# Kernel optimization log

Hardware: AMD Instinct MI355X
Metric: run time of the kernel (lower is better)

## Reference

```python
import jax, jax.numpy as jnp
import numpy as np

N = 100_000      # nodes
E = 500_000      # edges
D = 128          # node_feature_dim
IN = 2 * D       # VAE in_features
H = 128          # hidden_ch
L = 5            # latent_features
V2 = 3.5
BETA = 10.0


def _init_linear(key, fan_in, fan_out):
    kw, kb = jax.random.split(key)
    bound = 1.0 / np.sqrt(fan_in)
    W = jax.random.uniform(kw, (fan_in, fan_out), jnp.float32, -bound, bound)
    b = jax.random.uniform(kb, (fan_out,), jnp.float32, -bound, bound)
    return W, b


def setup_inputs() -> dict:
    key = jax.random.key(0)
    ks = jax.random.split(key, 12)
    x = jax.random.normal(ks[0], (N, D), jnp.float32)
    row = jax.random.randint(ks[1], (E,), 0, N, jnp.int32)
    col = jax.random.randint(ks[2], (E,), 0, N, jnp.int32)
    eps = jax.random.normal(ks[3], (E, L), jnp.float32)
    # encoder FCBlock: IN -> H -> H -> H -> 2L (ReLU on hidden layers)
    eW0, eb0 = _init_linear(ks[4], IN, H)
    eW1, eb1 = _init_linear(ks[5], H, H)
    eW2, eb2 = _init_linear(ks[6], H, H)
    eW3, eb3 = _init_linear(ks[7], H, 2 * L)
    # decoder FCBlock: L -> H -> H -> H -> IN
    dW0, db0 = _init_linear(ks[8], L, H)
    dW1, db1 = _init_linear(ks[9], H, H)
    dW2, db2 = _init_linear(ks[10], H, H)
    dW3, db3 = _init_linear(ks[11], H, IN)
    return dict(x=x, row=row, col=col, eps=eps,
                eW0=eW0, eb0=eb0, eW1=eW1, eb1=eb1, eW2=eW2, eb2=eb2, eW3=eW3, eb3=eb3,
                dW0=dW0, db0=db0, dW1=dW1, db1=db1, dW2=dW2, db2=db2, dW3=dW3, db3=db3)


def _mlp(h, layers):
    # ReLU on all but the last layer (FCBlock)
    n = len(layers)
    for i, (W, b) in enumerate(layers):
        h = h @ W + b
        if i < n - 1:
            h = jax.nn.relu(h)
    return h


def reference(x, row, col, eps,
              eW0, eb0, eW1, eb1, eW2, eb2, eW3, eb3,
              dW0, db0, dW1, db1, dW2, db2, dW3, db3):
    # gather node pairs -> [E, 2D]
    pair = jnp.concatenate([x[row], x[col]], axis=1)
    enc = _mlp(pair, [(eW0, eb0), (eW1, eb1), (eW2, eb2), (eW3, eb3)])
    mu, logvars = jnp.split(enc, 2, axis=1)          # [E, L] each
    std = jnp.exp(0.5 * logvars)
    z = mu + eps * std                               # reparameterization
    recon = _mlp(z, [(dW0, db0), (dW1, db1), (dW2, db2), (dW3, db3)])
    recon_loss = jnp.sqrt(jnp.sum((recon - pair) ** 2, axis=1))  # [E]
    kl_loss = -0.5 * (1.0 + logvars - mu ** 2 - jnp.exp(logvars)) * BETA  # [E, L]
    edge_affinities = 1.0 / (1.0 + V2 * recon_loss)  # [E]
    return edge_affinities, recon_loss.mean(), kl_loss.mean()
```

## Files before the change

### kernel.cpp

```cpp
#include <hip/hip_runtime.h>
#include <hip/hip_bf16.h>

typedef unsigned short u16;
typedef __attribute__((ext_vector_type(8))) short bf16x8;
typedef __attribute__((ext_vector_type(4))) float f32x4;

#define NE 500000
#define NBLOCKS ((NE + 127) / 128)

#define WE0_U 0u
#define WE1_U 32768u
#define WE2_U 49152u
#define WE3_U 65536u
#define WD0_U 67584u
#define WD1_U 71680u
#define WD2_U 88064u
#define WD3_U 104448u
#define WEND_U 137216u
#define BIAS_F 68608u
#define BE0_F 0
#define BE1_F 128
#define BE2_F 256
#define BE3_F 384
#define BD0_F 400
#define BD1_F 528
#define BD2_F 656
#define BD3_F 784
#define NBIAS 1040
#define ACC_BYTE 278592u

__device__ __forceinline__ u16 f2bf(float f) {
  __hip_bfloat16 h = __float2bfloat16(f);
  u16 u;
  __builtin_memcpy(&u, &h, 2);
  return u;
}

__global__ void prep_kernel(const float* __restrict__ eW0, const float* __restrict__ eb0,
                            const float* __restrict__ eW1, const float* __restrict__ eb1,
                            const float* __restrict__ eW2, const float* __restrict__ eb2,
                            const float* __restrict__ eW3, const float* __restrict__ eb3,
                            const float* __restrict__ dW0, const float* __restrict__ db0,
                            const float* __restrict__ dW1, const float* __restrict__ db1,
                            const float* __restrict__ dW2, const float* __restrict__ db2,
                            const float* __restrict__ dW3, const float* __restrict__ db3,
                            u16* __restrict__ wsu) {
  int t = blockIdx.x * 256 + threadIdx.x;
  float* wsf = (float*)wsu;
  if (t < 32768) {
    int n = t >> 8, k = t & 255;
    wsu[WE0_U + n * 256 + k] = f2bf(eW0[k * 128 + n]);
  } else if (t < 49152) {
    int i = t - 32768, n = i >> 7, k = i & 127;
    wsu[WE1_U + n * 128 + k] = f2bf(eW1[k * 128 + n]);
  } else if (t < 65536) {
    int i = t - 49152, n = i >> 7, k = i & 127;
    wsu[WE2_U + n * 128 + k] = f2bf(eW2[k * 128 + n]);
  } else if (t < 67584) {
    int i = t - 65536, n = i >> 7, k = i & 127;
    wsu[WE3_U + n * 128 + k] = f2bf(n < 10 ? eW3[k * 10 + n] : 0.f);
  } else if (t < 71680) {
    int i = t - 67584, n = i >> 5, k = i & 31;
    wsu[WD0_U + n * 32 + k] = f2bf(k < 5 ? dW0[k * 128 + n] : 0.f);
  } else if (t < 88064) {
    int i = t - 71680, n = i >> 7, k = i & 127;
    wsu[WD1_U + n * 128 + k] = f2bf(dW1[k * 128 + n]);
  } else if (t < 104448) {
    int i = t - 88064, n = i >> 7, k = i & 127;
    wsu[WD2_U + n * 128 + k] = f2bf(dW2[k * 128 + n]);
  } else if (t < 137216) {
    int i = t - 104448, n = i >> 7, k = i & 127;
    wsu[WD3_U + n * 128 + k] = f2bf(dW3[k * 256 + n]);
  } else if (t < 137216 + NBIAS) {
    int i = t - 137216;
    float v;
    if (i < 128) v = eb0[i];
    else if (i < 256) v = eb1[i - 128];
    else if (i < 384) v = eb2[i - 256];
    else if (i < 400) v = (i - 384 < 10) ? eb3[i - 384] : 0.f;
    else if (i < 528) v = db0[i - 400];
    else if (i < 656) v = db1[i - 528];
    else if (i < 784) v = db2[i - 656];
    else v = db3[i - 784];
    wsf[BIAS_F + i] = v;
  } else if (t < 137216 + NBIAS + 2) {
    ((double*)((char*)wsu + ACC_BYTE))[t - 137216 - NBIAS] = 0.0;
  }
}

__device__ __forceinline__ bf16x8 ldA(const u16* buf, int row, int k) {
  int byte = (row * 256 + k * 2) ^ ((row & 7) << 4);
  return *(const bf16x8*)((const char*)buf + byte);
}

__device__ __forceinline__ void init_acc(f32x4 acc[2][8], const float* __restrict__ bias, int j) {
  #pragma unroll
  for (int n = 0; n < 8; ++n) {
    float b = bias[n * 16 + j];
    f32x4 v = {b, b, b, b};
    acc[0][n] = v;
    acc[1][n] = v;
  }
}

template<int LDW>
__device__ __forceinline__ void gemm_acc(const u16* __restrict__ inb, const u16* __restrict__ Wt,
                                         int k0, f32x4 acc[2][8], int rw, int g, int j) {
  #pragma unroll
  for (int kk = 0; kk < 4; ++kk) {
    int k = kk * 32 + g * 8;
    bf16x8 a0 = ldA(inb, rw + j, k);
    bf16x8 a1 = ldA(inb, rw + 16 + j, k);
    #pragma unroll
    for (int n = 0; n < 8; ++n) {
      bf16x8 b = *(const bf16x8*)(Wt + (n * 16 + j) * LDW + k0 + k);
      acc[0][n] = __builtin_amdgcn_mfma_f32_16x16x32_bf16(a0, b, acc[0][n], 0, 0, 0);
      acc[1][n] = __builtin_amdgcn_mfma_f32_16x16x32_bf16(a1, b, acc[1][n], 0, 0, 0);
    }
  }
}

__device__ __forceinline__ void store_act(const f32x4 acc[2][8], u16* outb, int rw, int g, int j,
                                          bool relu) {
  #pragma unroll
  for (int m = 0; m < 2; ++m)
    #pragma unroll
    for (int n = 0; n < 8; ++n)
      #pragma unroll
      for (int r = 0; r < 4; ++r) {
        float v = acc[m][n][r];
        if (relu) v = fmaxf(v, 0.f);
        int row = rw + m * 16 + g * 4 + r;
        int c = n * 16 + j;
        int byte = (row * 256 + c * 2) ^ ((row & 7) << 4);
        *(u16*)((char*)outb + byte) = f2bf(v);
      }
}

__device__ __forceinline__ void stage(const float* __restrict__ x, const int* __restrict__ idx,
                                      int e0, u16* buf, int tid) {
  int gg = tid >> 4;
  int jj = tid & 15;
  #pragma unroll
  for (int p = 0; p < 8; ++p) {
    int rl = p * 16 + gg;
    int e = e0 + rl;
    if (e >= NE) e = NE - 1;
    int node = idx[e];
    const f32x4* src = (const f32x4*)(x + (size_t)node * 128 + jj * 8);
    f32x4 v0 = src[0];
    f32x4 v1 = src[1];
    bf16x8 o;
    o[0] = (short)f2bf(v0[0]); o[1] = (short)f2bf(v0[1]);
    o[2] = (short)f2bf(v0[2]); o[3] = (short)f2bf(v0[3]);
    o[4] = (short)f2bf(v1[0]); o[5] = (short)f2bf(v1[1]);
    o[6] = (short)f2bf(v1[2]); o[7] = (short)f2bf(v1[3]);
    int byte = (rl * 256 + jj * 16) ^ ((rl & 7) << 4);
    *(bf16x8*)((char*)buf + byte) = o;
  }
}

__global__ __launch_bounds__(256, 2) void vae_kernel(
    const float* __restrict__ x, const int* __restrict__ rowi, const int* __restrict__ coli,
    const float* __restrict__ eps, const u16* __restrict__ wsu, double* __restrict__ accg,
    float* __restrict__ out) {
  __shared__ __align__(16) u16 bufA[128 * 128];
  __shared__ __align__(16) u16 bufB[128 * 128];
  __shared__ __align__(16) u16 zbuf[128 * 32];
  __shared__ float redr[4], redk[4];

  const float* wsf = (const float*)wsu;
  const int tid = threadIdx.x;
  const int lane = tid & 63;
  const int wave = tid >> 6;
  const int g = lane >> 4;
  const int j = lane & 15;
  const int rw = wave * 32;
  const int e0 = blockIdx.x * 128;

  for (int i = tid; i < 128 * 32; i += 256) zbuf[i] = 0;

  float kl_part = 0.f, rl_part = 0.f;
  f32x4 acc[2][8];

  stage(x, rowi, e0, bufA, tid);
  __syncthreads();
  init_acc(acc, wsf + BIAS_F + BE0_F, j);
  gemm_acc<256>(bufA, wsu + WE0_U, 0, acc, rw, g, j);
  __syncthreads();
  stage(x, coli, e0, bufA, tid);
  __syncthreads();
  gemm_acc<256>(bufA, wsu + WE0_U, 128, acc, rw, g, j);
  store_act(acc, bufB, rw, g, j, true);
  __syncthreads();

  init_acc(acc, wsf + BIAS_F + BE1_F, j);
  gemm_acc<128>(bufB, wsu + WE1_U, 0, acc, rw, g, j);
  store_act(acc, bufA, rw, g, j, true);
  __syncthreads();

  init_acc(acc, wsf + BIAS_F + BE2_F, j);
  gemm_acc<128>(bufA, wsu + WE2_U, 0, acc, rw, g, j);
  store_act(acc, bufB, rw, g, j, true);
  __syncthreads();

  f32x4 a3[2];
  {
    float b3 = wsf[BIAS_F + BE3_F + j];
    f32x4 v = {b3, b3, b3, b3};
    a3[0] = v;
    a3[1] = v;
    #pragma unroll
    for (int kk = 0; kk < 4; ++kk) {
      int k = kk * 32 + g * 8;
      bf16x8 q0 = ldA(bufB, rw + j, k);
      bf16x8 q1 = ldA(bufB, rw + 16 + j, k);
      bf16x8 b = *(const bf16x8*)(wsu + WE3_U + j * 128 + k);
      a3[0] = __builtin_amdgcn_mfma_f32_16x16x32_bf16(q0, b, a3[0], 0, 0, 0);
      a3[1] = __builtin_amdgcn_mfma_f32_16x16x32_bf16(q1, b, a3[1], 0, 0, 0);
    }
  }

  {
    int src = g * 16 + ((j + 5) & 15);
    #pragma unroll
    for (int m = 0; m < 2; ++m)
      #pragma unroll
      for (int r = 0; r < 4; ++r) {
        float muv = a3[m][r];
        float lvv = __shfl(a3[m][r], src, 64);
        if (j < 5) {
          int row = rw + m * 16 + g * 4 + r;
          int e = e0 + row;
          int ec = e < NE ? e : NE - 1;
          float stdv = __expf(0.5f * lvv);
          float zv = muv + eps[(size_t)ec * 5 + j] * stdv;
          zbuf[row * 32 + j] = f2bf(zv);
          if (e < NE) kl_part += 1.0f + lvv - muv * muv - __expf(lvv);
        }
      }
  }
  __syncthreads();

  init_acc(acc, wsf + BIAS_F + BD0_F, j);
  {
    int k = g * 8;
    bf16x8 q0 = *(const bf16x8*)(zbuf + (rw + j) * 32 + k);
    bf16x8 q1 = *(const bf16x8*)(zbuf + (rw + 16 + j) * 32 + k);
    #pragma unroll
    for (int n = 0; n < 8; ++n) {
      bf16x8 b = *(const bf16x8*)(wsu + WD0_U + (n * 16 + j) * 32 + k);
      acc[0][n] = __builtin_amdgcn_mfma_f32_16x16x32_bf16(q0, b, acc[0][n], 0, 0, 0);
      acc[1][n] = __builtin_amdgcn_mfma_f32_16x16x32_bf16(q1, b, acc[1][n], 0, 0, 0);
    }
  }
  store_act(acc, bufA, rw, g, j, true);
  __syncthreads();

  init_acc(acc, wsf + BIAS_F + BD1_F, j);
  gemm_acc<128>(bufA, wsu + WD1_U, 0, acc, rw, g, j);
  store_act(acc, bufB, rw, g, j, true);
  __syncthreads();

  init_acc(acc, wsf + BIAS_F + BD2_F, j);
  gemm_acc<128>(bufB, wsu + WD2_U, 0, acc, rw, g, j);
  store_act(acc, bufA, rw, g, j, true);
  __syncthreads();

  int rn[2][4], cn[2][4];
  #pragma unroll
  for (int m = 0; m < 2; ++m)
    #pragma unroll
    for (int r = 0; r < 4; ++r) {
      int e = e0 + rw + m * 16 + g * 4 + r;
      int ec = e < NE ? e : NE - 1;
      rn[m][r] = rowi[ec];
      cn[m][r] = coli[ec];
    }
  float rlsq[2][4] = {{0.f, 0.f, 0.f, 0.f}, {0.f, 0.f, 0.f, 0.f}};
  #pragma unroll
  for (int nh = 0; nh < 2; ++nh) {
    init_acc(acc, wsf + BIAS_F + BD3_F + nh * 128, j);
    #pragma unroll
    for (int kk = 0; kk < 4; ++kk) {
      int k = kk * 32 + g * 8;
      bf16x8 q0 = ldA(bufA, rw + j, k);
      bf16x8 q1 = ldA(bufA, rw + 16 + j, k);
      #pragma unroll
      for (int n = 0; n < 8; ++n) {
        bf16x8 b = *(const bf16x8*)(wsu + WD3_U + (nh * 128 + n * 16 + j) * 128 + k);
        acc[0][n] = __builtin_amdgcn_mfma_f32_16x16x32_bf16(q0, b, acc[0][n], 0, 0, 0);
        acc[1][n] = __builtin_amdgcn_mfma_f32_16x16x32_bf16(q1, b, acc[1][n], 0, 0, 0);
      }
    }
    #pragma unroll
    for (int m = 0; m < 2; ++m)
      #pragma unroll
      for (int n = 0; n < 8; ++n)
        #pragma unroll
        for (int r = 0; r < 4; ++r) {
          int c = nh * 128 + n * 16 + j;
          int node = (c < 128) ? rn[m][r] : cn[m][r];
          float pv = x[(size_t)node * 128 + (c & 127)];
          float d = acc[m][n][r] - pv;
          rlsq[m][r] += d * d;
        }
  }

  #pragma unroll
  for (int m = 0; m < 2; ++m)
    #pragma unroll
    for (int r = 0; r < 4; ++r) {
      float v = rlsq[m][r];
      v += __shfl_xor(v, 1);
      v += __shfl_xor(v, 2);
      v += __shfl_xor(v, 4);
      v += __shfl_xor(v, 8);
      if (j == 0) {
        int e = e0 + rw + m * 16 + g * 4 + r;
        if (e < NE) {
          float rl = sqrtf(v);
          out[e] = 1.0f / (1.0f + 3.5f * rl);
          rl_part += rl;
        }
      }
    }

  float kv = kl_part, rv = rl_part;
  #pragma unroll
  for (int msk = 1; msk < 64; msk <<= 1) {
    kv += __shfl_xor(kv, msk);
    rv += __shfl_xor(rv, msk);
  }
  if (lane == 0) {
    redk[wave] = kv;
    redr[wave] = rv;
  }
  __syncthreads();
  if (tid == 0) {
    atomicAdd(&accg[0], (double)(redr[0] + redr[1] + redr[2] + redr[3]));
    atomicAdd(&accg[1], (double)(redk[0] + redk[1] + redk[2] + redk[3]));
  }
}

__global__ void fin_kernel(const double* __restrict__ accg, float* __restrict__ out) {
  if (threadIdx.x == 0) {
    out[NE] = (float)(accg[0] / (double)NE);
    out[NE + 1] = (float)(accg[1] * (-0.5 * 10.0 / ((double)NE * 5.0)));
  }
}

extern "C" void kernel_launch(void* const* d_in, const int* in_sizes, int n_in,
                              void* d_out, int out_size, void* d_ws, size_t ws_size,
                              hipStream_t stream) {
  (void)in_sizes; (void)n_in; (void)out_size; (void)ws_size;
  const float* x   = (const float*)d_in[0];
  const int*   row = (const int*)d_in[1];
  const int*   col = (const int*)d_in[2];
  const float* eps = (const float*)d_in[3];
  u16* wsu = (u16*)d_ws;
  double* accg = (double*)((char*)d_ws + ACC_BYTE);
  float* out = (float*)d_out;

  prep_kernel<<<541, 256, 0, stream>>>(
      (const float*)d_in[4],  (const float*)d_in[5],  (const float*)d_in[6],  (const float*)d_in[7],
      (const float*)d_in[8],  (const float*)d_in[9],  (const float*)d_in[10], (const float*)d_in[11],
      (const float*)d_in[12], (const float*)d_in[13], (const float*)d_in[14], (const float*)d_in[15],
      (const float*)d_in[16], (const float*)d_in[17], (const float*)d_in[18], (const float*)d_in[19],
      wsu);
  vae_kernel<<<NBLOCKS, 256, 0, stream>>>(x, row, col, eps, wsu, accg, out);
  fin_kernel<<<1, 64, 0, stream>>>(accg, out);
}
```

Before: 847.7 us.

## Halve edge tile to 64 rows per block to raise occupancy

Each block now processes 64 edges instead of 128, with each wave owning 16 rows and a single accumulator set, so registers and LDS per block are halved and launch bounds allow 4 blocks per SM. Staging now loads the row and column gathers into separate buffers before a single barrier, and each thread gathers contiguous 128-byte chunks of one node row. Row and column indices are loaded earlier. In exchange, B-fragment (weight) loads are amortised over half as many MFMAs, which raises weight-fetch traffic per edge.

```diff
diff --git a/kernel.cpp b/kernel.cpp
--- a/kernel.cpp
+++ b/kernel.cpp
@@ -6,7 +6,7 @@
 typedef __attribute__((ext_vector_type(4))) float f32x4;
 
 #define NE 500000
-#define NBLOCKS ((NE + 127) / 128)
+#define NBLOCKS ((NE + 63) / 64)
 
 #define WE0_U 0u
 #define WE1_U 32768u
@@ -16,7 +16,6 @@
 #define WD1_U 71680u
 #define WD2_U 88064u
 #define WD3_U 104448u
-#define WEND_U 137216u
 #define BIAS_F 68608u
 #define BE0_F 0
 #define BE1_F 128
@@ -93,80 +92,75 @@
   return *(const bf16x8*)((const char*)buf + byte);
 }
 
-__device__ __forceinline__ void init_acc(f32x4 acc[2][8], const float* __restrict__ bias, int j) {
+__device__ __forceinline__ void init_acc(f32x4 acc[8], const float* __restrict__ bias, int j) {
   #pragma unroll
   for (int n = 0; n < 8; ++n) {
     float b = bias[n * 16 + j];
     f32x4 v = {b, b, b, b};
-    acc[0][n] = v;
-    acc[1][n] = v;
+    acc[n] = v;
   }
 }
 
 template<int LDW>
 __device__ __forceinline__ void gemm_acc(const u16* __restrict__ inb, const u16* __restrict__ Wt,
-                                         int k0, f32x4 acc[2][8], int rw, int g, int j) {
+                                         int k0, f32x4 acc[8], int rw, int g, int j) {
   #pragma unroll
   for (int kk = 0; kk < 4; ++kk) {
     int k = kk * 32 + g * 8;
     bf16x8 a0 = ldA(inb, rw + j, k);
-    bf16x8 a1 = ldA(inb, rw + 16 + j, k);
     #pragma unroll
     for (int n = 0; n < 8; ++n) {
       bf16x8 b = *(const bf16x8*)(Wt + (n * 16 + j) * LDW + k0 + k);
-      acc[0][n] = __builtin_amdgcn_mfma_f32_16x16x32_bf16(a0, b, acc[0][n], 0, 0, 0);
-      acc[1][n] = __builtin_amdgcn_mfma_f32_16x16x32_bf16(a1, b, acc[1][n], 0, 0, 0);
-    }
-  }
-}
-
-__device__ __forceinline__ void store_act(const f32x4 acc[2][8], u16* outb, int rw, int g, int j,
+      acc[n] = __builtin_amdgcn_mfma_f32_16x16x32_bf16(a0, b, acc[n], 0, 0, 0);
+    }
+  }
+}
+
+__device__ __forceinline__ void store_act(const f32x4 acc[8], u16* outb, int rw, int g, int j,
                                           bool relu) {
   #pragma unroll
-  for (int m = 0; m < 2; ++m)
-    #pragma unroll
-    for (int n = 0; n < 8; ++n)
-      #pragma unroll
-      for (int r = 0; r < 4; ++r) {
-        float v = acc[m][n][r];
-        if (relu) v = fmaxf(v, 0.f);
-        int row = rw + m * 16 + g * 4 + r;
-        int c = n * 16 + j;
-        int byte = (row * 256 + c * 2) ^ ((row & 7) << 4);
-        *(u16*)((char*)outb + byte) = f2bf(v);
-      }
+  for (int n = 0; n < 8; ++n)
+    #pragma unroll
+    for (int r = 0; r < 4; ++r) {
+      float v = acc[n][r];
+      if (relu) v = fmaxf(v, 0.f);
+      int row = rw + g * 4 + r;
+      int c = n * 16 + j;
+      int byte = (row * 256 + c * 2) ^ ((row & 7) << 4);
+      *(u16*)((char*)outb + byte) = f2bf(v);
+    }
 }
 
 __device__ __forceinline__ void stage(const float* __restrict__ x, const int* __restrict__ idx,
                                       int e0, u16* buf, int tid) {
-  int gg = tid >> 4;
-  int jj = tid & 15;
-  #pragma unroll
-  for (int p = 0; p < 8; ++p) {
-    int rl = p * 16 + gg;
-    int e = e0 + rl;
-    if (e >= NE) e = NE - 1;
-    int node = idx[e];
-    const f32x4* src = (const f32x4*)(x + (size_t)node * 128 + jj * 8);
-    f32x4 v0 = src[0];
-    f32x4 v1 = src[1];
+  int rl = tid >> 2;
+  int sub = tid & 3;
+  int e = e0 + rl;
+  if (e >= NE) e = NE - 1;
+  int node = idx[e];
+  const f32x4* src = (const f32x4*)(x + (size_t)node * 128 + sub * 32);
+  #pragma unroll
+  for (int c = 0; c < 4; ++c) {
+    f32x4 v0 = src[c * 2];
+    f32x4 v1 = src[c * 2 + 1];
     bf16x8 o;
     o[0] = (short)f2bf(v0[0]); o[1] = (short)f2bf(v0[1]);
     o[2] = (short)f2bf(v0[2]); o[3] = (short)f2bf(v0[3]);
     o[4] = (short)f2bf(v1[0]); o[5] = (short)f2bf(v1[1]);
     o[6] = (short)f2bf(v1[2]); o[7] = (short)f2bf(v1[3]);
-    int byte = (rl * 256 + jj * 16) ^ ((rl & 7) << 4);
+    int col = sub * 32 + c * 8;
+    int byte = (rl * 256 + col * 2) ^ ((rl & 7) << 4);
     *(bf16x8*)((char*)buf + byte) = o;
   }
 }
 
-__global__ __launch_bounds__(256, 2) void vae_kernel(
+__global__ __launch_bounds__(256, 4) void vae_kernel(
     const float* __restrict__ x, const int* __restrict__ rowi, const int* __restrict__ coli,
     const float* __restrict__ eps, const u16* __restrict__ wsu, double* __restrict__ accg,
     float* __restrict__ out) {
-  __shared__ __align__(16) u16 bufA[128 * 128];
-  __shared__ __align__(16) u16 bufB[128 * 128];
-  __shared__ __align__(16) u16 zbuf[128 * 32];
+  __shared__ __align__(16) u16 bufA[64 * 128];
+  __shared__ __align__(16) u16 bufB[64 * 128];
+  __shared__ __align__(16) u16 zbuf[64 * 32];
   __shared__ float redr[4], redk[4];
 
   const float* wsf = (const float*)wsu;
@@ -175,70 +169,74 @@
   const int wave = tid >> 6;
   const int g = lane >> 4;
   const int j = lane & 15;
-  const int rw = wave * 32;
-  const int e0 = blockIdx.x * 128;
-
-  for (int i = tid; i < 128 * 32; i += 256) zbuf[i] = 0;
+  const int rw = wave * 16;
+  const int e0 = blockIdx.x * 64;
+
+  for (int i = tid; i < 64 * 32; i += 256) zbuf[i] = 0;
 
   float kl_part = 0.f, rl_part = 0.f;
-  f32x4 acc[2][8];
+  f32x4 acc[8];
 
   stage(x, rowi, e0, bufA, tid);
-  __syncthreads();
+  stage(x, coli, e0, bufB, tid);
+  __syncthreads();
+
   init_acc(acc, wsf + BIAS_F + BE0_F, j);
   gemm_acc<256>(bufA, wsu + WE0_U, 0, acc, rw, g, j);
-  __syncthreads();
-  stage(x, coli, e0, bufA, tid);
-  __syncthreads();
-  gemm_acc<256>(bufA, wsu + WE0_U, 128, acc, rw, g, j);
+  gemm_acc<256>(bufB, wsu + WE0_U, 128, acc, rw, g, j);
+  __syncthreads();
+  store_act(acc, bufA, rw, g, j, true);
+  __syncthreads();
+
+  init_acc(acc, wsf + BIAS_F + BE1_F, j);
+  gemm_acc<128>(bufA, wsu + WE1_U, 0, acc, rw, g, j);
   store_act(acc, bufB, rw, g, j, true);
   __syncthreads();
 
-  init_acc(acc, wsf + BIAS_F + BE1_F, j);
-  gemm_acc<128>(bufB, wsu + WE1_U, 0, acc, rw, g, j);
+  init_acc(acc, wsf + BIAS_F + BE2_F, j);
+  gemm_acc<128>(bufB, wsu + WE2_U, 0, acc, rw, g, j);
   store_act(acc, bufA, rw, g, j, true);
   __syncthreads();
 
-  init_acc(acc, wsf + BIAS_F + BE2_F, j);
-  gemm_acc<128>(bufA, wsu + WE2_U, 0, acc, rw, g, j);
-  store_act(acc, bufB, rw, g, j, true);
-  __syncthreads();
-
-  f32x4 a3[2];
+  f32x4 a3;
   {
     float b3 = wsf[BIAS_F + BE3_F + j];
     f32x4 v = {b3, b3, b3, b3};
-    a3[0] = v;
-    a3[1] = v;
+    a3 = v;
     #pragma unroll
     for (int kk = 0; kk < 4; ++kk) {
       int k = kk * 32 + g * 8;
-      bf16x8 q0 = ldA(bufB, rw + j, k);
-      bf16x8 q1 = ldA(bufB, rw + 16 + j, k);
+      bf16x8 q0 = ldA(bufA, rw + j, k);
       bf16x8 b = *(const bf16x8*)(wsu + WE3_U + j * 128 + k);
-      a3[0] = __builtin_amdgcn_mfma_f32_16x16x32_bf16(q0, b, a3[0], 0, 0, 0);
-      a3[1] = __builtin_amdgcn_mfma_f32_16x16x32_bf16(q1, b, a3[1], 0, 0, 0);
+      a3 = __builtin_amdgcn_mfma_f32_16x16x32_bf16(q0, b, a3, 0, 0, 0);
     }
   }
 
   {
     int src = g * 16 + ((j + 5) & 15);
     #pragma unroll
-    for (int m = 0; m < 2; ++m)
-      #pragma unroll
-      for (int r = 0; r < 4; ++r) {
-        float muv = a3[m][r];
-        float lvv = __shfl(a3[m][r], src, 64);
-        if (j < 5) {
-          int row = rw + m * 16 + g * 4 + r;
-          int e = e0 + row;
-          int ec = e < NE ? e : NE - 1;
-          float stdv = __expf(0.5f * lvv);
-          float zv = muv + eps[(size_t)ec * 5 + j] * stdv;
-          zbuf[row * 32 + j] = f2bf(zv);
-          if (e < NE) kl_part += 1.0f + lvv - muv * muv - __expf(lvv);
-        }
+    for (int r = 0; r < 4; ++r) {
+      float muv = a3[r];
+      float lvv = __shfl(a3[r], src, 64);
+      if (j < 5) {
+        int row = rw + g * 4 + r;
+        int e = e0 + row;
+        int ec = e < NE ? e : NE - 1;
+        float stdv = __expf(0.5f * lvv);
+        float zv = muv + eps[(size_t)ec * 5 + j] * stdv;
+        zbuf[row * 32 + j] = f2bf(zv);
+        if (e < NE) kl_part += 1.0f + lvv - muv * muv - __expf(lvv);
       }
+    }
+  }
+
+  int rn[4], cn[4];
+  #pragma unroll
+  for (int r = 0; r < 4; ++r) {
+    int e = e0 + rw + g * 4 + r;
+    int ec = e < NE ? e : NE - 1;
+    rn[r] = rowi[ec];
+    cn[r] = coli[ec];
   }
   __syncthreads();
 
@@ -246,85 +244,67 @@
   {
     int k = g * 8;
     bf16x8 q0 = *(const bf16x8*)(zbuf + (rw + j) * 32 + k);
-    bf16x8 q1 = *(const bf16x8*)(zbuf + (rw + 16 + j) * 32 + k);
     #pragma unroll
     for (int n = 0; n < 8; ++n) {
       bf16x8 b = *(const bf16x8*)(wsu + WD0_U + (n * 16 + j) * 32 + k);
-      acc[0][n] = __builtin_amdgcn_mfma_f32_16x16x32_bf16(q0, b, acc[0][n], 0, 0, 0);
-      acc[1][n] = __builtin_amdgcn_mfma_f32_16x16x32_bf16(q1, b, acc[1][n], 0, 0, 0);
-    }
-  }
+      acc[n] = __builtin_amdgcn_mfma_f32_16x16x32_bf16(q0, b, acc[n], 0, 0, 0);
+    }
+  }
+  store_act(acc, bufB, rw, g, j, true);
+  __syncthreads();
+
+  init_acc(acc, wsf + BIAS_F + BD1_F, j);
+  gemm_acc<128>(bufB, wsu + WD1_U, 0, acc, rw, g, j);
   store_act(acc, bufA, rw, g, j, true);
   __syncthreads();
 
-  init_acc(acc, wsf + BIAS_F + BD1_F, j);
-  gemm_acc<128>(bufA, wsu + WD1_U, 0, acc, rw, g, j);
+  init_acc(acc, wsf + BIAS_F + BD2_F, j);
+  gemm_acc<128>(bufA, wsu + WD2_U, 0, acc, rw, g, j);
   store_act(acc, bufB, rw, g, j, true);
   __syncthreads();
 
-  init_acc(acc, wsf + BIAS_F + BD2_F, j);
-  gemm_acc<128>(bufB, wsu + WD2_U, 0, acc, rw, g, j);
-  store_act(acc, bufA, rw, g, j, true);
-  __syncthreads();
-
-  int rn[2][4], cn[2][4];
-  #pragma unroll
-  for (int m = 0; m < 2; ++m)
-    #pragma unroll
-    for (int r = 0; r < 4; ++r) {
-      int e = e0 + rw + m * 16 + g * 4 + r;
-      int ec = e < NE ? e : NE - 1;
-      rn[m][r] = rowi[ec];
-      cn[m][r] = coli[ec];
-    }
-  float rlsq[2][4] = {{0.f, 0.f, 0.f, 0.f}, {0.f, 0.f, 0.f, 0.f}};
+  float rlsq[4] = {0.f, 0.f, 0.f, 0.f};
   #pragma unroll
   for (int nh = 0; nh < 2; ++nh) {
     init_acc(acc, wsf + BIAS_F + BD3_F + nh * 128, j);
     #pragma unroll
     for (int kk = 0; kk < 4; ++kk) {
       int k = kk * 32 + g * 8;
-      bf16x8 q0 = ldA(bufA, rw + j, k);
-      bf16x8 q1 = ldA(bufA, rw + 16 + j, k);
+      bf16x8 q0 = ldA(bufB, rw + j, k);
       #pragma unroll
       for (int n = 0; n < 8; ++n) {
         bf16x8 b = *(const bf16x8*)(wsu + WD3_U + (nh * 128 + n * 16 + j) * 128 + k);
-        acc[0][n] = __builtin_amdgcn_mfma_f32_16x16x32_bf16(q0, b, acc[0][n], 0, 0, 0);
-        acc[1][n] = __builtin_amdgcn_mfma_f32_16x16x32_bf16(q1, b, acc[1][n], 0, 0, 0);
+        acc[n] = __builtin_amdgcn_mfma_f32_16x16x32_bf16(q0, b, acc[n], 0, 0, 0);
       }
     }
     #pragma unroll
-    for (int m = 0; m < 2; ++m)
+    for (int n = 0; n < 8; ++n)
       #pragma unroll
-      for (int n = 0; n < 8; ++n)
-        #pragma unroll
-        for (int r = 0; r < 4; ++r) {
-          int c = nh * 128 + n * 16 + j;
-          int node = (c < 128) ? rn[m][r] : cn[m][r];
-          float pv = x[(size_t)node * 128 + (c & 127)];
-          float d = acc[m][n][r] - pv;
-          rlsq[m][r] += d * d;
-        }
-  }
-
-  #pragma unroll
-  for (int m = 0; m < 2; ++m)
-    #pragma unroll
-    for (int r = 0; r < 4; ++r) {
-      float v = rlsq[m][r];
-      v += __shfl_xor(v, 1);
-      v += __shfl_xor(v, 2);
-      v += __shfl_xor(v, 4);
-      v += __shfl_xor(v, 8);
-      if (j == 0) {
-        int e = e0 + rw + m * 16 + g * 4 + r;
-        if (e < NE) {
-          float rl = sqrtf(v);
-          out[e] = 1.0f / (1.0f + 3.5f * rl);
-          rl_part += rl;
-        }
+      for (int r = 0; r < 4; ++r) {
+        int c = nh * 128 + n * 16 + j;
+        int node = (nh == 0) ? rn[r] : cn[r];
+        float pv = x[(size_t)node * 128 + (c & 127)];
+        float d = acc[n][r] - pv;
+        rlsq[r] += d * d;
       }
-    }
+  }
+
+  #pragma unroll
+  for (int r = 0; r < 4; ++r) {
+    float v = rlsq[r];
+    v += __shfl_xor(v, 1);
+    v += __shfl_xor(v, 2);
+    v += __shfl_xor(v, 4);
+    v += __shfl_xor(v, 8);
+    if (j == 0) {
+      int e = e0 + rw + g * 4 + r;
+      if (e < NE) {
+        float rl = sqrtf(v);
+        out[e] = 1.0f / (1.0f + 3.5f * rl);
+        rl_part += rl;
+      }
+    }
+  }
 
   float kv = kl_part, rv = rl_part;
   #pragma unroll
```

New measurement: 1.218 ms. 1.44x slower.

## Make each wave own its rows, drop block barriers, and split accumulators

Applied to the files above, without the earlier changes.

Staging, z-buffer init and every layer now touch only the 32 rows owned by the current wave, so all __syncthreads between layers are removed. Row and column features are staged into two separate LDS buffers up front instead of reusing one buffer. Hidden and output layers now compute 64-column halves with a smaller accumulator array, to cut register pressure. The risk is that correctness depends on strictly wave-private LDS access. The split into halves also rereads the A operand from LDS once per half.

```diff
diff --git a/kernel.cpp b/kernel.cpp
--- a/kernel.cpp
+++ b/kernel.cpp
@@ -16,7 +16,6 @@
 #define WD1_U 71680u
 #define WD2_U 88064u
 #define WD3_U 104448u
-#define WEND_U 137216u
 #define BIAS_F 68608u
 #define BE0_F 0
 #define BE1_F 128
@@ -34,6 +33,11 @@
   u16 u;
   __builtin_memcpy(&u, &h, 2);
   return u;
+}
+
+__device__ __forceinline__ f32x4 bcast4(float b) {
+  f32x4 v = {b, b, b, b};
+  return v;
 }
 
 __global__ void prep_kernel(const float* __restrict__ eW0, const float* __restrict__ eb0,
@@ -93,69 +97,81 @@
   return *(const bf16x8*)((const char*)buf + byte);
 }
 
-__device__ __forceinline__ void init_acc(f32x4 acc[2][8], const float* __restrict__ bias, int j) {
-  #pragma unroll
-  for (int n = 0; n < 8; ++n) {
-    float b = bias[n * 16 + j];
-    f32x4 v = {b, b, b, b};
+__device__ __forceinline__ void init_half(f32x4 acc[2][4], const float* __restrict__ bias,
+                                          int nh, int j) {
+  #pragma unroll
+  for (int n = 0; n < 4; ++n) {
+    f32x4 v = bcast4(bias[nh * 64 + n * 16 + j]);
     acc[0][n] = v;
     acc[1][n] = v;
   }
 }
 
 template<int LDW>
-__device__ __forceinline__ void gemm_acc(const u16* __restrict__ inb, const u16* __restrict__ Wt,
-                                         int k0, f32x4 acc[2][8], int rw, int g, int j) {
+__device__ __forceinline__ void gemm_half(const u16* __restrict__ inb, const u16* __restrict__ Wt,
+                                          int k0, int nh, f32x4 acc[2][4], int rw, int g, int j) {
   #pragma unroll
   for (int kk = 0; kk < 4; ++kk) {
     int k = kk * 32 + g * 8;
     bf16x8 a0 = ldA(inb, rw + j, k);
     bf16x8 a1 = ldA(inb, rw + 16 + j, k);
     #pragma unroll
-    for (int n = 0; n < 8; ++n) {
-      bf16x8 b = *(const bf16x8*)(Wt + (n * 16 + j) * LDW + k0 + k);
+    for (int n = 0; n < 4; ++n) {
+      bf16x8 b = *(const bf16x8*)(Wt + ((nh * 4 + n) * 16 + j) * LDW + k0 + k);
       acc[0][n] = __builtin_amdgcn_mfma_f32_16x16x32_bf16(a0, b, acc[0][n], 0, 0, 0);
       acc[1][n] = __builtin_amdgcn_mfma_f32_16x16x32_bf16(a1, b, acc[1][n], 0, 0, 0);
     }
   }
 }
 
-__device__ __forceinline__ void store_act(const f32x4 acc[2][8], u16* outb, int rw, int g, int j,
-                                          bool relu) {
+__device__ __forceinline__ void store_half(const f32x4 acc[2][4], u16* outb, int rw, int nh,
+                                           int g, int j, bool relu) {
   #pragma unroll
   for (int m = 0; m < 2; ++m)
     #pragma unroll
-    for (int n = 0; n < 8; ++n)
+    for (int n = 0; n < 4; ++n)
       #pragma unroll
       for (int r = 0; r < 4; ++r) {
         float v = acc[m][n][r];
         if (relu) v = fmaxf(v, 0.f);
         int row = rw + m * 16 + g * 4 + r;
-        int c = n * 16 + j;
+        int c = nh * 64 + n * 16 + j;
         int byte = (row * 256 + c * 2) ^ ((row & 7) << 4);
         *(u16*)((char*)outb + byte) = f2bf(v);
       }
 }
 
+__device__ __forceinline__ void layer128(const u16* __restrict__ inb, u16* __restrict__ outb,
+                                         const u16* __restrict__ Wt, const float* __restrict__ bias,
+                                         int rw, int g, int j) {
+  #pragma unroll
+  for (int nh = 0; nh < 2; ++nh) {
+    f32x4 acc[2][4];
+    init_half(acc, bias, nh, j);
+    gemm_half<128>(inb, Wt, 0, nh, acc, rw, g, j);
+    store_half(acc, outb, rw, nh, g, j, true);
+  }
+}
+
 __device__ __forceinline__ void stage(const float* __restrict__ x, const int* __restrict__ idx,
-                                      int e0, u16* buf, int tid) {
-  int gg = tid >> 4;
-  int jj = tid & 15;
-  #pragma unroll
-  for (int p = 0; p < 8; ++p) {
-    int rl = p * 16 + gg;
-    int e = e0 + rl;
-    if (e >= NE) e = NE - 1;
-    int node = idx[e];
-    const f32x4* src = (const f32x4*)(x + (size_t)node * 128 + jj * 8);
-    f32x4 v0 = src[0];
-    f32x4 v1 = src[1];
+                                      int e0, u16* buf, int rw, int lane) {
+  int rl = rw + (lane >> 1);
+  int sub = lane & 1;
+  int e = e0 + rl;
+  if (e >= NE) e = NE - 1;
+  int node = idx[e];
+  const f32x4* src = (const f32x4*)(x + (size_t)node * 128 + sub * 64);
+  #pragma unroll
+  for (int c = 0; c < 8; ++c) {
+    f32x4 v0 = src[c * 2];
+    f32x4 v1 = src[c * 2 + 1];
     bf16x8 o;
     o[0] = (short)f2bf(v0[0]); o[1] = (short)f2bf(v0[1]);
     o[2] = (short)f2bf(v0[2]); o[3] = (short)f2bf(v0[3]);
     o[4] = (short)f2bf(v1[0]); o[5] = (short)f2bf(v1[1]);
     o[6] = (short)f2bf(v1[2]); o[7] = (short)f2bf(v1[3]);
-    int byte = (rl * 256 + jj * 16) ^ ((rl & 7) << 4);
+    int col = sub * 64 + c * 8;
+    int byte = (rl * 256 + col * 2) ^ ((rl & 7) << 4);
     *(bf16x8*)((char*)buf + byte) = o;
   }
 }
@@ -178,43 +194,78 @@
   const int rw = wave * 32;
   const int e0 = blockIdx.x * 128;
 
-  for (int i = tid; i < 128 * 32; i += 256) zbuf[i] = 0;
+  {
+    bf16x8 zz = {};
+    int zr = rw + (lane >> 1);
+    int zc = (lane & 1) * 16;
+    *(bf16x8*)(zbuf + zr * 32 + zc) = zz;
+    *(bf16x8*)(zbuf + zr * 32 + zc + 8) = zz;
+  }
 
   float kl_part = 0.f, rl_part = 0.f;
-  f32x4 acc[2][8];
-
-  stage(x, rowi, e0, bufA, tid);
-  __syncthreads();
-  init_acc(acc, wsf + BIAS_F + BE0_F, j);
-  gemm_acc<256>(bufA, wsu + WE0_U, 0, acc, rw, g, j);
-  __syncthreads();
-  stage(x, coli, e0, bufA, tid);
-  __syncthreads();
-  gemm_acc<256>(bufA, wsu + WE0_U, 128, acc, rw, g, j);
-  store_act(acc, bufB, rw, g, j, true);
-  __syncthreads();
-
-  init_acc(acc, wsf + BIAS_F + BE1_F, j);
-  gemm_acc<128>(bufB, wsu + WE1_U, 0, acc, rw, g, j);
-  store_act(acc, bufA, rw, g, j, true);
-  __syncthreads();
-
-  init_acc(acc, wsf + BIAS_F + BE2_F, j);
-  gemm_acc<128>(bufA, wsu + WE2_U, 0, acc, rw, g, j);
-  store_act(acc, bufB, rw, g, j, true);
-  __syncthreads();
+
+  stage(x, rowi, e0, bufA, rw, lane);
+  stage(x, coli, e0, bufB, rw, lane);
+
+  {
+    f32x4 acc8[2][8];
+    #pragma unroll
+    for (int n = 0; n < 8; ++n) {
+      f32x4 v = bcast4(wsf[BIAS_F + BE0_F + n * 16 + j]);
+      acc8[0][n] = v;
+      acc8[1][n] = v;
+    }
+    #pragma unroll
+    for (int kk = 0; kk < 4; ++kk) {
+      int k = kk * 32 + g * 8;
+      bf16x8 a0 = ldA(bufA, rw + j, k);
+      bf16x8 a1 = ldA(bufA, rw + 16 + j, k);
+      #pragma unroll
+      for (int n = 0; n < 8; ++n) {
+        bf16x8 b = *(const bf16x8*)(wsu + WE0_U + (n * 16 + j) * 256 + k);
+        acc8[0][n] = __builtin_amdgcn_mfma_f32_16x16x32_bf16(a0, b, acc8[0][n], 0, 0, 0);
+        acc8[1][n] = __builtin_amdgcn_mfma_f32_16x16x32_bf16(a1, b, acc8[1][n], 0, 0, 0);
+      }
+    }
+    #pragma unroll
+    for (int kk = 0; kk < 4; ++kk) {
+      int k = kk * 32 + g * 8;
+      bf16x8 a0 = ldA(bufB, rw + j, k);
+      bf16x8 a1 = ldA(bufB, rw + 16 + j, k);
+      #pragma unroll
+      for (int n = 0; n < 8; ++n) {
+        bf16x8 b = *(const bf16x8*)(wsu + WE0_U + (n * 16 + j) * 256 + 128 + k);
+        acc8[0][n] = __builtin_amdgcn_mfma_f32_16x16x32_bf16(a0, b, acc8[0][n], 0, 0, 0);
+        acc8[1][n] = __builtin_amdgcn_mfma_f32_16x16x32_bf16(a1, b, acc8[1][n], 0, 0, 0);
+      }
+    }
+    #pragma unroll
+    for (int m = 0; m < 2; ++m)
+      #pragma unroll
+      for (int n = 0; n < 8; ++n)
+        #pragma unroll
+        for (int r = 0; r < 4; ++r) {
+          float v = fmaxf(acc8[m][n][r], 0.f);
+          int row = rw + m * 16 + g * 4 + r;
+          int c = n * 16 + j;
+          int byte = (row * 256 + c * 2) ^ ((row & 7) << 4);
+          *(u16*)((char*)bufA + byte) = f2bf(v);
+        }
+  }
+
+  layer128(bufA, bufB, wsu + WE1_U, wsf + BIAS_F + BE1_F, rw, g, j);
+  layer128(bufB, bufA, wsu + WE2_U, wsf + BIAS_F + BE2_F, rw, g, j);
 
   f32x4 a3[2];
   {
-    float b3 = wsf[BIAS_F + BE3_F + j];
-    f32x4 v = {b3, b3, b3, b3};
+    f32x4 v = bcast4(wsf[BIAS_F + BE3_F + j]);
     a3[0] = v;
     a3[1] = v;
     #pragma unroll
     for (int kk = 0; kk < 4; ++kk) {
       int k = kk * 32 + g * 8;
-      bf16x8 q0 = ldA(bufB, rw + j, k);
-      bf16x8 q1 = ldA(bufB, rw + 16 + j, k);
+      bf16x8 q0 = ldA(bufA, rw + j, k);
+      bf16x8 q1 = ldA(bufA, rw + 16 + j, k);
       bf16x8 b = *(const bf16x8*)(wsu + WE3_U + j * 128 + k);
       a3[0] = __builtin_amdgcn_mfma_f32_16x16x32_bf16(q0, b, a3[0], 0, 0, 0);
       a3[1] = __builtin_amdgcn_mfma_f32_16x16x32_bf16(q1, b, a3[1], 0, 0, 0);
@@ -240,32 +291,25 @@
         }
       }
   }
-  __syncthreads();
-
-  init_acc(acc, wsf + BIAS_F + BD0_F, j);
-  {
+
+  #pragma unroll
+  for (int nh = 0; nh < 2; ++nh) {
+    f32x4 acc[2][4];
+    init_half(acc, wsf + BIAS_F + BD0_F, nh, j);
     int k = g * 8;
     bf16x8 q0 = *(const bf16x8*)(zbuf + (rw + j) * 32 + k);
     bf16x8 q1 = *(const bf16x8*)(zbuf + (rw + 16 + j) * 32 + k);
     #pragma unroll
-    for (int n = 0; n < 8; ++n) {
-      bf16x8 b = *(const bf16x8*)(wsu + WD0_U + (n * 16 + j) * 32 + k);
+    for (int n = 0; n < 4; ++n) {
+      bf16x8 b = *(const bf16x8*)(wsu + WD0_U + ((nh * 4 + n) * 16 + j) * 32 + k);
       acc[0][n] = __builtin_amdgcn_mfma_f32_16x16x32_bf16(q0, b, acc[0][n], 0, 0, 0);
       acc[1][n] = __builtin_amdgcn_mfma_f32_16x16x32_bf16(q1, b, acc[1][n], 0, 0, 0);
     }
-  }
-  store_act(acc, bufA, rw, g, j, true);
-  __syncthreads();
-
-  init_acc(acc, wsf + BIAS_F + BD1_F, j);
-  gemm_acc<128>(bufA, wsu + WD1_U, 0, acc, rw, g, j);
-  store_act(acc, bufB, rw, g, j, true);
-  __syncthreads();
-
-  init_acc(acc, wsf + BIAS_F + BD2_F, j);
-  gemm_acc<128>(bufB, wsu + WD2_U, 0, acc, rw, g, j);
-  store_act(acc, bufA, rw, g, j, true);
-  __syncthreads();
+    store_half(acc, bufB, rw, nh, g, j, true);
+  }
+
+  layer128(bufB, bufA, wsu + WD1_U, wsf + BIAS_F + BD1_F, rw, g, j);
+  layer128(bufA, bufB, wsu + WD2_U, wsf + BIAS_F + BD2_F, rw, g, j);
 
   int rn[2][4], cn[2][4];
   #pragma unroll
@@ -277,29 +321,20 @@
       rn[m][r] = rowi[ec];
       cn[m][r] = coli[ec];
     }
+
   float rlsq[2][4] = {{0.f, 0.f, 0.f, 0.f}, {0.f, 0.f, 0.f, 0.f}};
   #pragma unroll
-  for (int nh = 0; nh < 2; ++nh) {
-    init_acc(acc, wsf + BIAS_F + BD3_F + nh * 128, j);
-    #pragma unroll
-    for (int kk = 0; kk < 4; ++kk) {
-      int k = kk * 32 + g * 8;
-      bf16x8 q0 = ldA(bufA, rw + j, k);
-      bf16x8 q1 = ldA(bufA, rw + 16 + j, k);
-      #pragma unroll
-      for (int n = 0; n < 8; ++n) {
-        bf16x8 b = *(const bf16x8*)(wsu + WD3_U + (nh * 128 + n * 16 + j) * 128 + k);
-        acc[0][n] = __builtin_amdgcn_mfma_f32_16x16x32_bf16(q0, b, acc[0][n], 0, 0, 0);
-        acc[1][n] = __builtin_amdgcn_mfma_f32_16x16x32_bf16(q1, b, acc[1][n], 0, 0, 0);
-      }
-    }
+  for (int qh = 0; qh < 4; ++qh) {
+    f32x4 acc[2][4];
+    init_half(acc, wsf + BIAS_F + BD3_F, qh, j);
+    gemm_half<128>(bufB, wsu + WD3_U, 0, qh, acc, rw, g, j);
     #pragma unroll
     for (int m = 0; m < 2; ++m)
       #pragma unroll
-      for (int n = 0; n < 8; ++n)
+      for (int n = 0; n < 4; ++n)
         #pragma unroll
         for (int r = 0; r < 4; ++r) {
-          int c = nh * 128 + n * 16 + j;
+          int c = qh * 64 + n * 16 + j;
           int node = (c < 128) ? rn[m][r] : cn[m][r];
           float pv = x[(size_t)node * 128 + (c & 127)];
           float d = acc[m][n][r] - pv;
```

Result: faster. 801.6 us (-5.4%).
